# Performance work log

Hardware: AMD Instinct MI355X
Metric: run time of the kernel (lower is better)

The kernel has to match this reference:

```python
import jax, jax.numpy as jnp
import numpy as np

B, H, T, DH = 1, 16, 2048, 64
D = 64  # neighbors per query


def setup_inputs() -> dict:
    key = jax.random.key(0)
    k1, k2, k3, k4, k5, k6 = jax.random.split(key, 6)
    q = jax.random.normal(k1, (B, H, T, DH), dtype=jnp.float32)
    k = jax.random.normal(k2, (B, H, T, DH), dtype=jnp.float32)
    v = jax.random.normal(k3, (B, H, T, DH), dtype=jnp.float32)
    edge_type_bias = jax.random.normal(k4, (4,), dtype=jnp.float32) * 0.1
    neigh_idx = jax.random.randint(k5, (B, H, T, D), 0, T, dtype=jnp.int32)
    edge_type = jax.random.randint(k6, (B, H, T, D), 0, 5, dtype=jnp.int32)
    return {"q": q, "k": k, "v": v, "edge_type_bias": edge_type_bias,
            "neigh_idx": neigh_idx, "edge_type": edge_type}


def _gather_neighbors(x, idx):
    # x: [B,H,T,dh], idx: [B,H,T,D] -> [B,H,T,D,dh]
    return jax.vmap(jax.vmap(lambda xs, ii: xs[ii]))(x, idx)


def reference(q, k, v, edge_type_bias, neigh_idx, edge_type):
    b, h, t, dh = q.shape
    # safe_neighbor_idx: clamp out-of-range indices for the gather
    safe_idx = jnp.clip(neigh_idx, 0, t - 1)
    # causal_neighbor_mask: neighbor j valid iff 0 <= j <= i (original order)
    pos = jnp.arange(t, dtype=neigh_idx.dtype)[None, None, :, None]
    mask = (neigh_idx >= 0) & (neigh_idx <= pos)  # [B,H,T,D]
    k_g = _gather_neighbors(k, safe_idx)  # [B,H,T,D,dh]
    v_g = _gather_neighbors(v, safe_idx)  # [B,H,T,D,dh]
    scores = jnp.einsum('bhte,bhtde->bhtd', q, k_g) / jnp.sqrt(jnp.float32(dh))
    # edge-type bias: table [0, bias0..bias3] indexed by edge_type in {0..4}
    full_bias = jnp.concatenate([jnp.zeros((1,), jnp.float32), edge_type_bias])
    scores = scores + full_bias[edge_type]
    # stable masked softmax (fully-masked rows -> all-zero weights)
    neg = jnp.finfo(scores.dtype).min
    s = jnp.where(mask, scores, neg)
    m = jnp.max(s, axis=-1, keepdims=True)
    e = jnp.exp(s - m) * mask.astype(scores.dtype)
    denom = jnp.sum(e, axis=-1, keepdims=True)
    weights = e / jnp.maximum(denom, 1e-20)
    out = jnp.einsum('bhtd,bhtde->bhte', weights, v_g).astype(v.dtype)
    return out
```

## Files before the change

kernel.cpp:

```cpp
#include <hip/hip_runtime.h>
#include <hip/hip_fp16.h>
#include <math.h>


#define T_DIM 2048
#define DH    64
#define NB    64
#define WPB   2
#define KV_ELEMS (16 * T_DIM * DH)

typedef _Float16 h2_t __attribute__((ext_vector_type(2)));

__global__ __launch_bounds__(256)
void convert_kv_kernel(const float* __restrict__ k, const float* __restrict__ v,
                       unsigned int* __restrict__ ws)
{
    const int tid = blockIdx.x * 256 + threadIdx.x;
    unsigned int* kh = ws;
    unsigned int* vh = ws + (KV_ELEMS / 2);
    const float4 kv = *(const float4*)(k + (long long)tid * 4);
    const float4 vv = *(const float4*)(v + (long long)tid * 4);
    h2_t k0 = { (_Float16)kv.x, (_Float16)kv.y };
    h2_t k1 = { (_Float16)kv.z, (_Float16)kv.w };
    h2_t v0 = { (_Float16)vv.x, (_Float16)vv.y };
    h2_t v1 = { (_Float16)vv.z, (_Float16)vv.w };
    uint2 pk, pv;
    pk.x = __builtin_bit_cast(unsigned int, k0);
    pk.y = __builtin_bit_cast(unsigned int, k1);
    pv.x = __builtin_bit_cast(unsigned int, v0);
    pv.y = __builtin_bit_cast(unsigned int, v1);
    *(uint2*)(kh + tid * 2) = pk;
    *(uint2*)(vh + tid * 2) = pv;
}

__device__ __forceinline__ float f16lo(unsigned int u) {
    return __low2float(__builtin_bit_cast(__half2, u));
}
__device__ __forceinline__ float f16hi(unsigned int u) {
    return __high2float(__builtin_bit_cast(__half2, u));
}

__device__ __forceinline__ float dot2f(unsigned int ku, h2_t qh, float c) {
#if __has_builtin(__builtin_amdgcn_fdot2)
    return __builtin_amdgcn_fdot2(__builtin_bit_cast(h2_t, ku), qh, c, false);
#else
    return c + f16lo(ku) * (float)qh.x + f16hi(ku) * (float)qh.y;
#endif
}

__global__ __launch_bounds__(WPB * 64)
void wayfinder_attn_f16(const float* __restrict__ q,
                        const unsigned int* __restrict__ kvws,
                        const float* __restrict__ etb,
                        const int*   __restrict__ neigh_idx,
                        const int*   __restrict__ edge_type,
                        float*       __restrict__ out)
{
    __shared__ int   j_s[WPB][NB];
    __shared__ float b_s[WPB][NB];
    __shared__ float w_s[WPB][NB];
    __shared__ float dot_s[WPB][NB];

    const int lane = threadIdx.x & 63;
    const int wave = threadIdx.x >> 6;

    const int bid = blockIdx.x;
    const int swz = (bid & 7) * 2048 + (bid >> 3);

    const int wq   = swz * WPB + wave;
    const int t    = wq & (T_DIM - 1);
    const int qbase    = wq * DH;
    const int headbase = (wq - t) * DH;
    const unsigned int* __restrict__ kh = kvws + (headbase >> 1);
    const unsigned int* __restrict__ vh = kvws + (KV_ELEMS / 2) + (headbase >> 1);

    j_s[wave][lane] = 0;
    b_s[wave][lane] = 0.f;

    const int raw = neigh_idx[wq * NB + lane];
    const int et  = edge_type[wq * NB + lane];
    const bool valid = (raw >= 0) && (raw <= t);
    const int  sj    = min(max(raw, 0), T_DIM - 1);
    const float bias = (et != 0) ? etb[et - 1] : 0.f;

    const unsigned long long vb = __ballot(valid);
    const int nv  = __popcll(vb);
    const int pos = __popcll(vb & ((1ull << lane) - 1ull));
    if (valid) { j_s[wave][pos] = sj; b_s[wave][pos] = bias; }

    const int c8 = lane & 7;
    const int g8 = lane >> 3;
    const float4 qv0 = *(const float4*)(q + qbase + c8 * 8);
    const float4 qv1 = *(const float4*)(q + qbase + c8 * 8 + 4);
    const h2_t qh0 = { (_Float16)qv0.x, (_Float16)qv0.y };
    const h2_t qh1 = { (_Float16)qv0.z, (_Float16)qv0.w };
    const h2_t qh2 = { (_Float16)qv1.x, (_Float16)qv1.y };
    const h2_t qh3 = { (_Float16)qv1.z, (_Float16)qv1.w };

    uint4 kr[8];
    #pragma unroll
    for (int i = 0; i < 8; ++i) {
        if (i * 8 < nv) {
            const int je = j_s[wave][i * 8 + g8];
            kr[i] = *(const uint4*)(kh + je * 32 + c8 * 4);
        }
    }

    #pragma unroll
    for (int i = 0; i < 8; ++i) {
        if (i * 8 < nv) {
            const uint4 u = kr[i];
            float p = dot2f(u.x, qh0, 0.f);
            p = dot2f(u.y, qh1, p);
            p = dot2f(u.z, qh2, p);
            p = dot2f(u.w, qh3, p);
            p += __shfl_xor(p, 1, 64);
            p += __shfl_xor(p, 2, 64);
            p += __shfl_xor(p, 4, 64);
            if (c8 == 0) dot_s[wave][i * 8 + g8] = p;
        }
    }
    const float mydot = dot_s[wave][lane];

    const bool dval = lane < nv;
    const float score = dval ? (mydot * 0.125f + b_s[wave][lane]) : -INFINITY;
    float m = score;
    #pragma unroll
    for (int o = 32; o > 0; o >>= 1) m = fmaxf(m, __shfl_xor(m, o, 64));
    const float e = dval ? __expf(score - m) : 0.f;
    float s = e;
    #pragma unroll
    for (int o = 32; o > 0; o >>= 1) s += __shfl_xor(s, o, 64);
    const float w = e / fmaxf(s, 1e-20f);
    w_s[wave][lane] = w;

    const int qw   = lane >> 4;
    const int lp16 = lane & 15;
    float a0 = 0.f, a1 = 0.f, a2 = 0.f, a3 = 0.f;
    for (int base = 0; base < nv; base += 16) {
        const int eb = base + qw * 4;
        const int4   jd = *(const int4*)&j_s[wave][eb];
        const float4 wd = *(const float4*)&w_s[wave][eb];
        const uint2 u0 = *(const uint2*)(vh + jd.x * 32 + lp16 * 2);
        const uint2 u1 = *(const uint2*)(vh + jd.y * 32 + lp16 * 2);
        const uint2 u2 = *(const uint2*)(vh + jd.z * 32 + lp16 * 2);
        const uint2 u3 = *(const uint2*)(vh + jd.w * 32 + lp16 * 2);
        a0 += wd.x * f16lo(u0.x);  a1 += wd.x * f16hi(u0.x);
        a2 += wd.x * f16lo(u0.y);  a3 += wd.x * f16hi(u0.y);
        a0 += wd.y * f16lo(u1.x);  a1 += wd.y * f16hi(u1.x);
        a2 += wd.y * f16lo(u1.y);  a3 += wd.y * f16hi(u1.y);
        a0 += wd.z * f16lo(u2.x);  a1 += wd.z * f16hi(u2.x);
        a2 += wd.z * f16lo(u2.y);  a3 += wd.z * f16hi(u2.y);
        a0 += wd.w * f16lo(u3.x);  a1 += wd.w * f16hi(u3.x);
        a2 += wd.w * f16lo(u3.y);  a3 += wd.w * f16hi(u3.y);
    }
    a0 += __shfl_xor(a0, 16, 64);  a1 += __shfl_xor(a1, 16, 64);
    a2 += __shfl_xor(a2, 16, 64);  a3 += __shfl_xor(a3, 16, 64);
    a0 += __shfl_xor(a0, 32, 64);  a1 += __shfl_xor(a1, 32, 64);
    a2 += __shfl_xor(a2, 32, 64);  a3 += __shfl_xor(a3, 32, 64);
    if (lane < 16) {
        float4 o; o.x = a0; o.y = a1; o.z = a2; o.w = a3;
        *(float4*)(out + qbase + lane * 4) = o;
    }
}

__global__ __launch_bounds__(256)
void wayfinder_attn_f32(const float* __restrict__ q,
                        const float* __restrict__ k,
                        const float* __restrict__ v,
                        const float* __restrict__ etb,
                        const int*   __restrict__ neigh_idx,
                        const int*   __restrict__ edge_type,
                        float*       __restrict__ out)
{
    __shared__ int   j_s[4][NB];
    __shared__ float w_s[4][NB];

    const int lane = threadIdx.x & 63;
    const int wave = threadIdx.x >> 6;
    const int wq   = blockIdx.x * 4 + wave;
    const int t    = wq & (T_DIM - 1);
    const long long qbase    = (long long)wq * DH;
    const long long headbase = (long long)(wq - t) * DH;

    const long long nbase = (long long)wq * NB;
    const int raw = neigh_idx[nbase + lane];
    const int et  = edge_type[nbase + lane];
    const bool valid = (raw >= 0) && (raw <= t);
    const int  sj   = min(max(raw, 0), T_DIM - 1);
    j_s[wave][lane] = sj;

    const int c = lane & 15;
    const int g = lane >> 4;
    const float4 qv = *(const float4*)(q + qbase + c * 4);

    int jarr[16];
    {
        const int4* jg = (const int4*)&j_s[wave][g * 16];
        *(int4*)&jarr[0]  = jg[0];
        *(int4*)&jarr[4]  = jg[1];
        *(int4*)&jarr[8]  = jg[2];
        *(int4*)&jarr[12] = jg[3];
    }

    const float* __restrict__ khead = k + headbase;
    float mydot = 0.f;
    #pragma unroll
    for (int i = 0; i < 16; ++i) {
        const float4 kv = *(const float4*)(khead + (long long)jarr[i] * DH + c * 4);
        float p = kv.x * qv.x + kv.y * qv.y + kv.z * qv.z + kv.w * qv.w;
        p += __shfl_xor(p, 1, 64);
        p += __shfl_xor(p, 2, 64);
        p += __shfl_xor(p, 4, 64);
        p += __shfl_xor(p, 8, 64);
        if (c == i) mydot = p;
    }

    const float bias  = (et != 0) ? etb[et - 1] : 0.f;
    const float score = valid ? (mydot * 0.125f + bias) : -INFINITY;

    float m = score;
    #pragma unroll
    for (int o = 32; o > 0; o >>= 1) m = fmaxf(m, __shfl_xor(m, o, 64));
    const float e = valid ? __expf(score - m) : 0.f;
    float s = e;
    #pragma unroll
    for (int o = 32; o > 0; o >>= 1) s += __shfl_xor(s, o, 64);
    const float w = e / fmaxf(s, 1e-20f);
    w_s[wave][lane] = w;

    const float* __restrict__ vhead = v + headbase;
    float acc = 0.f;
    #pragma unroll
    for (int d4 = 0; d4 < 16; ++d4) {
        const float4 wd = *(const float4*)&w_s[wave][d4 * 4];
        const int4   jd = *(const int4*)&j_s[wave][d4 * 4];
        acc += wd.x * vhead[(long long)jd.x * DH + lane];
        acc += wd.y * vhead[(long long)jd.y * DH + lane];
        acc += wd.z * vhead[(long long)jd.z * DH + lane];
        acc += wd.w * vhead[(long long)jd.w * DH + lane];
    }
    out[qbase + lane] = acc;
}

extern "C" void kernel_launch(void* const* d_in, const int* in_sizes, int n_in,
                              void* d_out, int out_size, void* d_ws, size_t ws_size,
                              hipStream_t stream)
{
    const float* q   = (const float*)d_in[0];
    const float* k   = (const float*)d_in[1];
    const float* v   = (const float*)d_in[2];
    const float* etb = (const float*)d_in[3];
    const int* neigh_idx = (const int*)d_in[4];
    const int* edge_type = (const int*)d_in[5];
    float* out = (float*)d_out;

    const int total_queries = 16 * T_DIM;
    const size_t need = (size_t)KV_ELEMS * 2 * sizeof(unsigned short);

    if (ws_size >= need) {
        unsigned int* ws = (unsigned int*)d_ws;
        hipLaunchKernelGGL(convert_kv_kernel, dim3(KV_ELEMS / 4 / 256), dim3(256),
                           0, stream, k, v, ws);
        hipLaunchKernelGGL(wayfinder_attn_f16, dim3(total_queries / WPB),
                           dim3(WPB * 64), 0, stream,
                           q, ws, etb, neigh_idx, edge_type, out);
    } else {
        hipLaunchKernelGGL(wayfinder_attn_f32, dim3(total_queries / 4), dim3(256),
                           0, stream, q, k, v, etb, neigh_idx, edge_type, out);
    }
}
```

Before: 111.0 us.

## Keep scores in registers and prefetch V gathers alongside K in f16 attention

Restructures the per-query wave so the dot products stay in registers with the same 8-lane-per-neighbor layout used for K. V rows are issued as uint4 gathers right after the K dot products, before the softmax runs. The softmax is then done over registers with cross-group shuffles, and the weighted V sum reuses that layout. This removes the dot_s/w_s shared-memory round trips and the serial V gather loop, and overlaps V memory latency with the softmax. The cost is more live registers (kr, vr, p, ex arrays), which could reduce occupancy.

```diff
diff --git a/kernel.cpp b/kernel.cpp
--- a/kernel.cpp
+++ b/kernel.cpp
@@ -58,8 +58,6 @@
 {
     __shared__ int   j_s[WPB][NB];
     __shared__ float b_s[WPB][NB];
-    __shared__ float w_s[WPB][NB];
-    __shared__ float dot_s[WPB][NB];
 
     const int lane = threadIdx.x & 63;
     const int wave = threadIdx.x >> 6;
@@ -90,6 +88,7 @@
 
     const int c8 = lane & 7;
     const int g8 = lane >> 3;
+
     const float4 qv0 = *(const float4*)(q + qbase + c8 * 8);
     const float4 qv1 = *(const float4*)(q + qbase + c8 * 8 + 4);
     const h2_t qh0 = { (_Float16)qv0.x, (_Float16)qv0.y };
@@ -97,70 +96,90 @@
     const h2_t qh2 = { (_Float16)qv1.x, (_Float16)qv1.y };
     const h2_t qh3 = { (_Float16)qv1.z, (_Float16)qv1.w };
 
+    int je[8];
+    #pragma unroll
+    for (int i = 0; i < 8; ++i) je[i] = j_s[wave][i * 8 + g8];
+
     uint4 kr[8];
     #pragma unroll
     for (int i = 0; i < 8; ++i) {
-        if (i * 8 < nv) {
-            const int je = j_s[wave][i * 8 + g8];
-            kr[i] = *(const uint4*)(kh + je * 32 + c8 * 4);
-        }
-    }
-
-    #pragma unroll
-    for (int i = 0; i < 8; ++i) {
+        if (i * 8 < nv) kr[i] = *(const uint4*)(kh + je[i] * 32 + c8 * 4);
+    }
+
+    float p[8];
+    #pragma unroll
+    for (int i = 0; i < 8; ++i) {
+        p[i] = 0.f;
         if (i * 8 < nv) {
             const uint4 u = kr[i];
-            float p = dot2f(u.x, qh0, 0.f);
-            p = dot2f(u.y, qh1, p);
-            p = dot2f(u.z, qh2, p);
-            p = dot2f(u.w, qh3, p);
-            p += __shfl_xor(p, 1, 64);
-            p += __shfl_xor(p, 2, 64);
-            p += __shfl_xor(p, 4, 64);
-            if (c8 == 0) dot_s[wave][i * 8 + g8] = p;
+            float d = dot2f(u.x, qh0, 0.f);
+            d = dot2f(u.y, qh1, d);
+            d = dot2f(u.z, qh2, d);
+            d = dot2f(u.w, qh3, d);
+            d += __shfl_xor(d, 1, 64);
+            d += __shfl_xor(d, 2, 64);
+            d += __shfl_xor(d, 4, 64);
+            p[i] = d;
         }
     }
-    const float mydot = dot_s[wave][lane];
-
-    const bool dval = lane < nv;
-    const float score = dval ? (mydot * 0.125f + b_s[wave][lane]) : -INFINITY;
-    float m = score;
-    #pragma unroll
-    for (int o = 32; o > 0; o >>= 1) m = fmaxf(m, __shfl_xor(m, o, 64));
-    const float e = dval ? __expf(score - m) : 0.f;
-    float s = e;
-    #pragma unroll
-    for (int o = 32; o > 0; o >>= 1) s += __shfl_xor(s, o, 64);
-    const float w = e / fmaxf(s, 1e-20f);
-    w_s[wave][lane] = w;
-
-    const int qw   = lane >> 4;
-    const int lp16 = lane & 15;
+
+    uint4 vr[8];
+    #pragma unroll
+    for (int i = 0; i < 8; ++i) {
+        if (i * 8 < nv) vr[i] = *(const uint4*)(vh + je[i] * 32 + c8 * 4);
+    }
+
+    float sc[8];
+    #pragma unroll
+    for (int i = 0; i < 8; ++i) {
+        const int e = i * 8 + g8;
+        sc[i] = (e < nv) ? (p[i] * 0.125f + b_s[wave][e]) : -INFINITY;
+    }
+    float m = sc[0];
+    #pragma unroll
+    for (int i = 1; i < 8; ++i) m = fmaxf(m, sc[i]);
+    m = fmaxf(m, __shfl_xor(m, 8, 64));
+    m = fmaxf(m, __shfl_xor(m, 16, 64));
+    m = fmaxf(m, __shfl_xor(m, 32, 64));
+
+    float ex[8];
+    float ssum = 0.f;
+    #pragma unroll
+    for (int i = 0; i < 8; ++i) {
+        const int e = i * 8 + g8;
+        ex[i] = (e < nv) ? __expf(sc[i] - m) : 0.f;
+        ssum += ex[i];
+    }
+    ssum += __shfl_xor(ssum, 8, 64);
+    ssum += __shfl_xor(ssum, 16, 64);
+    ssum += __shfl_xor(ssum, 32, 64);
+    const float inv = 1.f / fmaxf(ssum, 1e-20f);
+
     float a0 = 0.f, a1 = 0.f, a2 = 0.f, a3 = 0.f;
-    for (int base = 0; base < nv; base += 16) {
-        const int eb = base + qw * 4;
-        const int4   jd = *(const int4*)&j_s[wave][eb];
-        const float4 wd = *(const float4*)&w_s[wave][eb];
-        const uint2 u0 = *(const uint2*)(vh + jd.x * 32 + lp16 * 2);
-        const uint2 u1 = *(const uint2*)(vh + jd.y * 32 + lp16 * 2);
-        const uint2 u2 = *(const uint2*)(vh + jd.z * 32 + lp16 * 2);
-        const uint2 u3 = *(const uint2*)(vh + jd.w * 32 + lp16 * 2);
-        a0 += wd.x * f16lo(u0.x);  a1 += wd.x * f16hi(u0.x);
-        a2 += wd.x * f16lo(u0.y);  a3 += wd.x * f16hi(u0.y);
-        a0 += wd.y * f16lo(u1.x);  a1 += wd.y * f16hi(u1.x);
-        a2 += wd.y * f16lo(u1.y);  a3 += wd.y * f16hi(u1.y);
-        a0 += wd.z * f16lo(u2.x);  a1 += wd.z * f16hi(u2.x);
-        a2 += wd.z * f16lo(u2.y);  a3 += wd.z * f16hi(u2.y);
-        a0 += wd.w * f16lo(u3.x);  a1 += wd.w * f16hi(u3.x);
-        a2 += wd.w * f16lo(u3.y);  a3 += wd.w * f16hi(u3.y);
-    }
-    a0 += __shfl_xor(a0, 16, 64);  a1 += __shfl_xor(a1, 16, 64);
-    a2 += __shfl_xor(a2, 16, 64);  a3 += __shfl_xor(a3, 16, 64);
-    a0 += __shfl_xor(a0, 32, 64);  a1 += __shfl_xor(a1, 32, 64);
-    a2 += __shfl_xor(a2, 32, 64);  a3 += __shfl_xor(a3, 32, 64);
-    if (lane < 16) {
-        float4 o; o.x = a0; o.y = a1; o.z = a2; o.w = a3;
-        *(float4*)(out + qbase + lane * 4) = o;
+    float a4 = 0.f, a5 = 0.f, a6 = 0.f, a7 = 0.f;
+    #pragma unroll
+    for (int i = 0; i < 8; ++i) {
+        if (i * 8 < nv) {
+            const float w = ex[i] * inv;
+            const uint4 u = vr[i];
+            a0 += w * f16lo(u.x);  a1 += w * f16hi(u.x);
+            a2 += w * f16lo(u.y);  a3 += w * f16hi(u.y);
+            a4 += w * f16lo(u.z);  a5 += w * f16hi(u.z);
+            a6 += w * f16lo(u.w);  a7 += w * f16hi(u.w);
+        }
+    }
+    #pragma unroll
+    for (int off = 8; off <= 32; off <<= 1) {
+        a0 += __shfl_xor(a0, off, 64);  a1 += __shfl_xor(a1, off, 64);
+        a2 += __shfl_xor(a2, off, 64);  a3 += __shfl_xor(a3, off, 64);
+        a4 += __shfl_xor(a4, off, 64);  a5 += __shfl_xor(a5, off, 64);
+        a6 += __shfl_xor(a6, off, 64);  a7 += __shfl_xor(a7, off, 64);
+    }
+    if (g8 == 0) {
+        float4 o0; o0.x = a0; o0.y = a1; o0.z = a2; o0.w = a3;
+        float4 o1; o1.x = a4; o1.y = a5; o1.z = a6; o1.w = a7;
+        *(float4*)(out + qbase + c8 * 8)     = o0;
+        *(float4*)(out + qbase + c8 * 8 + 4) = o1;
     }
 }
 
```

Measured after the change: 120.5 us. 1.09x slower.
